# Kernel optimization log

Hardware: AMD Instinct MI355X
Metric: run time of the kernel (lower is better)

The kernel has to match this reference:

```python
import jax, jax.numpy as jnp
import numpy as np
from jax import lax

THD = 0.8  # Lowe ratio-test threshold (module init kwarg `thd`)


def setup_inputs() -> dict:
    key = jax.random.key(0)
    k1, k2 = jax.random.split(key)
    desc1 = jax.random.normal(k1, (16384, 128), dtype=jnp.float32)
    desc2 = jax.random.normal(k2, (16384, 128), dtype=jnp.float32)
    return {"desc1": desc1, "desc2": desc2}


def _cdist(a, b):
    # Euclidean pairwise distances, (B1, B2), same math as torch.cdist(p=2)
    sq_a = jnp.sum(a * a, axis=-1, keepdims=True)          # (B1, 1)
    sq_b = jnp.sum(b * b, axis=-1)                          # (B2,)
    d2 = sq_a + sq_b - 2.0 * (a @ b.T)                      # (B1, B2)
    return jnp.sqrt(jnp.maximum(d2, 0.0))


def reference(desc1, desc2):
    cost = _cdist(desc1, desc2)                             # (B1, B2)
    # two smallest distances per row
    neg_vals, idxs_in_2 = lax.top_k(-cost, 2)               # (B1, 2) each
    vals = -neg_vals
    ratio = vals[:, 0] / vals[:, 1]                         # (B1,)
    mask = ratio <= THD                                     # (B1,) bool
    # jit-compatible padded outputs: masked-out rows carry 0 distance; the
    # boolean mask selects the valid (idxs_in1, idxs_in2) match rows, which is
    # the compaction torch does with boolean indexing.
    match_dists = jnp.where(mask, ratio, 0.0)               # (B1,)
    idxs_in1 = jnp.arange(desc1.shape[0], dtype=jnp.int32)
    matches_idxs = jnp.stack([idxs_in1, idxs_in_2[:, 0].astype(jnp.int32)], axis=1)  # (B1, 2)
    return match_dists, matches_idxs, mask
```

## Files before the change

### kernel.cpp

```cpp
#include <hip/hip_runtime.h>
#include <math.h>
#include <float.h>
#include <stdint.h>


typedef __attribute__((ext_vector_type(4))) float     f32x4;
typedef __attribute__((ext_vector_type(8))) _Float16  half8;

#define D_     128
#define BM_    256
#define BN_    32
#define CS_    8
#define PARTS_ 8

__device__ __forceinline__ void gload_lds16(const void* g, void* l) {
  auto gp = (const __attribute__((address_space(1))) unsigned int*)(uintptr_t)g;
  auto lp = (__attribute__((address_space(3))) unsigned int*)(uintptr_t)l;
  __builtin_amdgcn_global_load_lds(gp, lp, 16, 0, 0);
}

__global__ void convert_kernel(const float* __restrict__ d1, const float* __restrict__ d2,
                               _Float16* __restrict__ Ahi, _Float16* __restrict__ Alo,
                               _Float16* __restrict__ BhiP, _Float16* __restrict__ BloP,
                               float* __restrict__ sq, int B) {
  int i = blockIdx.x * blockDim.x + threadIdx.x;
  int total = B * 16;
  if (i >= 2 * total) return;
  bool isB = i >= total;
  int j    = isB ? i - total : i;
  int desc = j >> 4;
  int seg  = j & 15;
  const float* src = (isB ? d2 : d1) + (size_t)desc * D_ + seg * 8;
  float4 v0 = *(const float4*)(src);
  float4 v1 = *(const float4*)(src + 4);
  half8 hv, lv;
  float e[8] = {v0.x, v0.y, v0.z, v0.w, v1.x, v1.y, v1.z, v1.w};
  float ss = 0.f;
  #pragma unroll
  for (int q = 0; q < 8; ++q) {
    ss = fmaf(e[q], e[q], ss);
    _Float16 h = (_Float16)e[q];
    _Float16 l = (_Float16)(e[q] - (float)h);
    if (isB) { h = (_Float16)(-2.0f) * h; l = (_Float16)(-2.0f) * l; }
    hv[q] = h; lv[q] = l;
  }
  #pragma unroll
  for (int off = 8; off > 0; off >>= 1) ss += __shfl_xor(ss, off, 64);
  if (seg == 0) sq[(isB ? B : 0) + desc] = ss;

  if (!isB) {
    *(half8*)(Ahi + (size_t)desc * D_ + seg * 8) = hv;
    *(half8*)(Alo + (size_t)desc * D_ + seg * 8) = lv;
  } else {
    int t   = desc >> 5, cloc = desc & 31;
    int nf  = cloc >> 4, c15  = cloc & 15;
    int kk  = seg >> 2,  gq   = seg & 3;
    size_t off = (size_t)t * 4096 + kk * 1024 + nf * 512 + gq * 128 + c15 * 8;
    *(half8*)(BhiP + off) = hv;
    *(half8*)(BloP + off) = lv;
  }
}

__global__ __launch_bounds__(256, 2)
void nn_mfma(const _Float16* __restrict__ Ahi, const _Float16* __restrict__ Alo,
             const _Float16* __restrict__ BhiP, const _Float16* __restrict__ BloP,
             const float* __restrict__ sqb,
             float* __restrict__ p_d0, float* __restrict__ p_d1,
             int* __restrict__ p_j0, int B) {
  extern __shared__ char smem[];
  float* sq_lds = (float*)(smem + 65536);
  const int tid  = threadIdx.x;
  const int lane = tid & 63;
  const int wid  = tid >> 6;
  const int l15  = lane & 15;
  const int g    = lane >> 4;

  const int nrb   = B / BM_;
  const int rb    = blockIdx.x % nrb;
  const int cspl  = blockIdx.x / nrb;
  const int i0    = rb * BM_;
  const int ntile = (B / CS_) / BN_;
  const int tile0 = cspl * ntile;

  half8 ah[4][4], al[4][4];
  #pragma unroll
  for (int mf = 0; mf < 4; ++mf) {
    int row = i0 + wid * 64 + mf * 16 + l15;
    const _Float16* pa = Ahi + (size_t)row * D_ + g * 8;
    const _Float16* pl = Alo + (size_t)row * D_ + g * 8;
    #pragma unroll
    for (int kk = 0; kk < 4; ++kk) {
      ah[mf][kk] = *(const half8*)(pa + kk * 32);
      al[mf][kk] = *(const half8*)(pl + kk * 32);
    }
  }

  {
    const float* sqs = sqb + cspl * 2048;
    #pragma unroll
    for (int e = 0; e < 2; ++e) {
      int idx = tid + e * 256;
      float4 v = ((const float4*)sqs)[idx];
      ((float4*)sq_lds)[idx] = v;
    }
  }

  const _Float16* srcW = ((wid < 2) ? BhiP : BloP)
                       + (size_t)tile0 * 4096 + (wid & 1) * 2048 + lane * 8;
  char* ldsW = smem + (wid >> 1) * 8192 + (wid & 1) * 4096;
  auto stage = [&](int slotbase, int t) {
    const _Float16* s = srcW + (size_t)t * 4096;
    char* l = ldsW + slotbase;
    #pragma unroll
    for (int e = 0; e < 4; ++e) gload_lds16(s + e * 512, l + e * 1024);
  };

  float best0[16], best1[16]; int bj[16];
  #pragma unroll
  for (int s = 0; s < 16; ++s) { best0[s] = FLT_MAX; best1[s] = FLT_MAX; bj[s] = 0x7fffffff; }

  const int colg0 = tile0 * BN_ + l15;

  auto tilecomp = [&](int t, int sb) {
    float sjc0 = sq_lds[t * 32 + l15];
    float sjc1 = sq_lds[t * 32 + 16 + l15];
    f32x4 acc[4][2];
    __builtin_amdgcn_s_setprio(1);
    #pragma unroll
    for (int kk = 0; kk < 4; ++kk) {
      half8 bh[2], bl[2];
      #pragma unroll
      for (int nf = 0; nf < 2; ++nf) {
        bh[nf] = *(const half8*)(smem + sb + kk * 2048 + nf * 1024 + lane * 16);
        bl[nf] = *(const half8*)(smem + sb + 8192 + kk * 2048 + nf * 1024 + lane * 16);
      }
      #pragma unroll
      for (int mf = 0; mf < 4; ++mf)
        #pragma unroll
        for (int nf = 0; nf < 2; ++nf) {
          if (kk == 0) {
            float sj = nf ? sjc1 : sjc0;
            f32x4 c0 = {sj, sj, sj, sj};
            acc[mf][nf] = __builtin_amdgcn_mfma_f32_16x16x32_f16(ah[mf][0], bh[nf], c0, 0, 0, 0);
          } else {
            acc[mf][nf] = __builtin_amdgcn_mfma_f32_16x16x32_f16(ah[mf][kk], bh[nf], acc[mf][nf], 0, 0, 0);
          }
        }
      #pragma unroll
      for (int mf = 0; mf < 4; ++mf)
        #pragma unroll
        for (int nf = 0; nf < 2; ++nf)
          acc[mf][nf] = __builtin_amdgcn_mfma_f32_16x16x32_f16(ah[mf][kk], bl[nf], acc[mf][nf], 0, 0, 0);
      #pragma unroll
      for (int mf = 0; mf < 4; ++mf)
        #pragma unroll
        for (int nf = 0; nf < 2; ++nf)
          acc[mf][nf] = __builtin_amdgcn_mfma_f32_16x16x32_f16(al[mf][kk], bh[nf], acc[mf][nf], 0, 0, 0);
    }
    __builtin_amdgcn_s_setprio(0);

    #pragma unroll
    for (int nf = 0; nf < 2; ++nf) {
      int colg = colg0 + t * BN_ + nf * 16;
      #pragma unroll
      for (int mf = 0; mf < 4; ++mf)
        #pragma unroll
        for (int r = 0; r < 4; ++r) {
          int s = mf * 4 + r;
          float v = acc[mf][nf][r];
          best1[s] = __builtin_amdgcn_fmed3f(v, best0[s], best1[s]);
          bool lt0 = v < best0[s];
          best0[s] = fminf(v, best0[s]);
          bj[s]    = lt0 ? colg : bj[s];
        }
    }
  };

  stage(0, 0);
  stage(16384, 1);
  asm volatile("s_waitcnt vmcnt(0)" ::: "memory");
  asm volatile("s_waitcnt lgkmcnt(0)" ::: "memory");
  __builtin_amdgcn_s_barrier();
  asm volatile("" ::: "memory");

  const int nper = ntile / 2;
  for (int p = 0; p < nper; ++p) {
    const int sbcur = (p & 1) * 32768;
    if (p + 1 < nper) {
      stage(sbcur ^ 32768, 2 * p + 2);
      stage((sbcur ^ 32768) + 16384, 2 * p + 3);
    }

    tilecomp(2 * p,     sbcur);
    tilecomp(2 * p + 1, sbcur + 16384);

    asm volatile("s_waitcnt vmcnt(0)" ::: "memory");
    __builtin_amdgcn_s_barrier();
    asm volatile("" ::: "memory");
  }

  #pragma unroll
  for (int off = 1; off < 16; off <<= 1) {
    #pragma unroll
    for (int s = 0; s < 16; ++s) {
      float e0 = __shfl_xor(best0[s], off, 64);
      float e1 = __shfl_xor(best1[s], off, 64);
      int   f0 = __shfl_xor(bj[s],    off, 64);
      if (e0 < best0[s] || (e0 == best0[s] && f0 < bj[s])) {
        best1[s] = fminf(best0[s], e1);
        best0[s] = e0;
        bj[s]    = f0;
      } else {
        best1[s] = fminf(best1[s], e0);
      }
    }
  }

  if (l15 == 0) {
    #pragma unroll
    for (int s = 0; s < 16; ++s) {
      int mf = s >> 2, r = s & 3;
      int row = i0 + wid * 64 + mf * 16 + g * 4 + r;
      p_d0[row * PARTS_ + cspl] = best0[s];
      p_d1[row * PARTS_ + cspl] = best1[s];
      p_j0[row * PARTS_ + cspl] = bj[s];
    }
  }
}

__global__ void nn_final(const float* __restrict__ sqa,
                         const float* __restrict__ p_d0,
                         const float* __restrict__ p_d1,
                         const int* __restrict__ p_j0,
                         float* __restrict__ out, int B) {
  int row = blockIdx.x * blockDim.x + threadIdx.x;
  if (row >= B) return;
  float d0 = FLT_MAX, d1 = FLT_MAX;
  int j0 = 0x7fffffff;
  for (int cs = 0; cs < PARTS_; ++cs) {
    float e0 = p_d0[row * PARTS_ + cs];
    float e1 = p_d1[row * PARTS_ + cs];
    int   f0 = p_j0[row * PARTS_ + cs];
    if (e0 < d0 || (e0 == d0 && f0 < j0)) {
      d1 = fminf(d0, e1);
      d0 = e0;
      j0 = f0;
    } else {
      d1 = fminf(d1, e0);
    }
  }
  float sa = sqa[row];
  float v0 = sqrtf(fmaxf(sa + d0, 0.f));
  float v1 = sqrtf(fmaxf(sa + d1, 0.f));
  float ratio = v0 / v1;
  bool m = (ratio <= 0.8f);
  out[row]             = m ? ratio : 0.f;
  out[B + row * 2]     = (float)row;
  out[B + row * 2 + 1] = (float)j0;
  out[3 * B + row]     = m ? 1.f : 0.f;
}

extern "C" void kernel_launch(void* const* d_in, const int* in_sizes, int n_in,
                              void* d_out, int out_size, void* d_ws, size_t ws_size,
                              hipStream_t stream) {
  const float* d1 = (const float*)d_in[0];
  const float* d2 = (const float*)d_in[1];
  const int B = in_sizes[0] / D_;

  float* ws   = (float*)d_ws;
  float* sqa  = ws;
  float* sqb  = ws + B;
  float* p_d0 = ws + 2 * B;
  float* p_d1 = ws + 10 * B;
  int*   p_j0 = (int*)(ws + 18 * B);
  _Float16* Ahi  = (_Float16*)(ws + 26 * B);
  _Float16* Alo  = Ahi + (size_t)B * D_;
  _Float16* BhiP = Alo + (size_t)B * D_;
  _Float16* BloP = BhiP + (size_t)B * D_;

  int ngroups = 2 * B * 16;
  convert_kernel<<<(ngroups + 255) / 256, 256, 0, stream>>>(d1, d2, Ahi, Alo, BhiP, BloP, sqa, B);

  hipFuncSetAttribute((const void*)nn_mfma,
                      hipFuncAttributeMaxDynamicSharedMemorySize, 73728);
  nn_mfma<<<(B / BM_) * CS_, 256, 73728, stream>>>(Ahi, Alo, BhiP, BloP, sqb,
                                                   p_d0, p_d1, p_j0, B);

  nn_final<<<(B + 255) / 256, 256, 0, stream>>>(sqa, p_d0, p_d1, p_j0, (float*)d_out, B);
}
```

Baseline: 173.9 us.

## Use triple-buffered single-tile LDS pipeline and load half of B-lo directly

Moves from double-buffered pairs of tiles to a three-slot ring of single tiles, prefetching two tiles ahead and waiting on partial vmcnt rather than draining all loads. Only 12 KB per tile is staged through LDS; the upper half of the B-lo fragments is read straight from global memory into registers each iteration. LDS use per block drops from 72 KB to 44 KB, which leaves room for more resident blocks per CU. The trade-off is an extra global load in the inner loop that may stall, and correctness now depends on the vmcnt(3) accounting matching three async loads per stage.

```diff
diff --git a/kernel.cpp b/kernel.cpp
--- a/kernel.cpp
+++ b/kernel.cpp
@@ -68,7 +68,7 @@
              float* __restrict__ p_d0, float* __restrict__ p_d1,
              int* __restrict__ p_j0, int B) {
   extern __shared__ char smem[];
-  float* sq_lds = (float*)(smem + 65536);
+  float* sq_lds = (float*)(smem + 36864);
   const int tid  = threadIdx.x;
   const int lane = tid & 63;
   const int wid  = tid >> 6;
@@ -79,8 +79,8 @@
   const int rb    = blockIdx.x % nrb;
   const int cspl  = blockIdx.x / nrb;
   const int i0    = rb * BM_;
-  const int ntile = (B / CS_) / BN_;
-  const int tile0 = cspl * ntile;
+  const int niter = (B / CS_) / BN_;
+  const int tile0 = cspl * niter;
 
   half8 ah[4][4], al[4][4];
   #pragma unroll
@@ -105,14 +105,15 @@
     }
   }
 
-  const _Float16* srcW = ((wid < 2) ? BhiP : BloP)
-                       + (size_t)tile0 * 4096 + (wid & 1) * 2048 + lane * 8;
-  char* ldsW = smem + (wid >> 1) * 8192 + (wid & 1) * 4096;
   auto stage = [&](int slotbase, int t) {
-    const _Float16* s = srcW + (size_t)t * 4096;
-    char* l = ldsW + slotbase;
-    #pragma unroll
-    for (int e = 0; e < 4; ++e) gload_lds16(s + e * 512, l + e * 1024);
+    const size_t tb = (size_t)(tile0 + t) * 4096;
+    #pragma unroll
+    for (int e = 0; e < 3; ++e) {
+      int c = wid * 3 + e;
+      const _Float16* s = (c < 8) ? (BhiP + tb + c * 512 + lane * 8)
+                                  : (BloP + tb + (c - 8) * 512 + lane * 8);
+      gload_lds16(s, smem + slotbase + c * 1024);
+    }
   };
 
   float best0[16], best1[16]; int bj[16];
@@ -121,9 +122,28 @@
 
   const int colg0 = tile0 * BN_ + l15;
 
-  auto tilecomp = [&](int t, int sb) {
-    float sjc0 = sq_lds[t * 32 + l15];
-    float sjc1 = sq_lds[t * 32 + 16 + l15];
+  stage(0, 0);
+  stage(12288, 1);
+  asm volatile("s_waitcnt vmcnt(3)" ::: "memory");
+  asm volatile("s_waitcnt lgkmcnt(0)" ::: "memory");
+  __builtin_amdgcn_s_barrier();
+  asm volatile("" ::: "memory");
+
+  int bcur = 0, bstage = 24576;
+  for (int it = 0; it < niter; ++it) {
+    const _Float16* blsrc = BloP + (size_t)(tile0 + it) * 4096 + lane * 8;
+    half8 blr[2][2];
+    #pragma unroll
+    for (int dk = 0; dk < 2; ++dk)
+      #pragma unroll
+      for (int nf = 0; nf < 2; ++nf)
+        blr[dk][nf] = *(const half8*)(blsrc + (2 + dk) * 1024 + nf * 512);
+
+    if (it + 2 < niter) stage(bstage, it + 2);
+
+    float sjc0 = sq_lds[it * 32 + l15];
+    float sjc1 = sq_lds[it * 32 + 16 + l15];
+
     f32x4 acc[4][2];
     __builtin_amdgcn_s_setprio(1);
     #pragma unroll
@@ -131,8 +151,11 @@
       half8 bh[2], bl[2];
       #pragma unroll
       for (int nf = 0; nf < 2; ++nf) {
-        bh[nf] = *(const half8*)(smem + sb + kk * 2048 + nf * 1024 + lane * 16);
-        bl[nf] = *(const half8*)(smem + sb + 8192 + kk * 2048 + nf * 1024 + lane * 16);
+        bh[nf] = *(const half8*)(smem + bcur + (kk * 2 + nf) * 1024 + lane * 16);
+        if (kk < 2)
+          bl[nf] = *(const half8*)(smem + bcur + 8192 + (kk * 2 + nf) * 1024 + lane * 16);
+        else
+          bl[nf] = blr[kk - 2][nf];
       }
       #pragma unroll
       for (int mf = 0; mf < 4; ++mf)
@@ -161,42 +184,27 @@
 
     #pragma unroll
     for (int nf = 0; nf < 2; ++nf) {
-      int colg = colg0 + t * BN_ + nf * 16;
+      int colg = colg0 + it * BN_ + nf * 16;
       #pragma unroll
       for (int mf = 0; mf < 4; ++mf)
         #pragma unroll
         for (int r = 0; r < 4; ++r) {
           int s = mf * 4 + r;
-          float v = acc[mf][nf][r];
-          best1[s] = __builtin_amdgcn_fmed3f(v, best0[s], best1[s]);
-          bool lt0 = v < best0[s];
-          best0[s] = fminf(v, best0[s]);
+          float t = acc[mf][nf][r];
+          best1[s] = __builtin_amdgcn_fmed3f(t, best0[s], best1[s]);
+          bool lt0 = t < best0[s];
+          best0[s] = fminf(t, best0[s]);
           bj[s]    = lt0 ? colg : bj[s];
         }
     }
-  };
-
-  stage(0, 0);
-  stage(16384, 1);
-  asm volatile("s_waitcnt vmcnt(0)" ::: "memory");
-  asm volatile("s_waitcnt lgkmcnt(0)" ::: "memory");
-  __builtin_amdgcn_s_barrier();
-  asm volatile("" ::: "memory");
-
-  const int nper = ntile / 2;
-  for (int p = 0; p < nper; ++p) {
-    const int sbcur = (p & 1) * 32768;
-    if (p + 1 < nper) {
-      stage(sbcur ^ 32768, 2 * p + 2);
-      stage((sbcur ^ 32768) + 16384, 2 * p + 3);
-    }
-
-    tilecomp(2 * p,     sbcur);
-    tilecomp(2 * p + 1, sbcur + 16384);
-
-    asm volatile("s_waitcnt vmcnt(0)" ::: "memory");
+
+    if (it + 2 < niter) asm volatile("s_waitcnt vmcnt(3)" ::: "memory");
+    else                asm volatile("s_waitcnt vmcnt(0)" ::: "memory");
     __builtin_amdgcn_s_barrier();
     asm volatile("" ::: "memory");
+
+    bcur   = (bcur   == 24576) ? 0 : bcur   + 12288;
+    bstage = (bstage == 24576) ? 0 : bstage + 12288;
   }
 
   #pragma unroll
@@ -282,8 +290,8 @@
   convert_kernel<<<(ngroups + 255) / 256, 256, 0, stream>>>(d1, d2, Ahi, Alo, BhiP, BloP, sqa, B);
 
   hipFuncSetAttribute((const void*)nn_mfma,
-                      hipFuncAttributeMaxDynamicSharedMemorySize, 73728);
-  nn_mfma<<<(B / BM_) * CS_, 256, 73728, stream>>>(Ahi, Alo, BhiP, BloP, sqb,
+                      hipFuncAttributeMaxDynamicSharedMemorySize, 45056);
+  nn_mfma<<<(B / BM_) * CS_, 256, 45056, stream>>>(Ahi, Alo, BhiP, BloP, sqb,
                                                    p_d0, p_d1, p_j0, B);
 
   nn_final<<<(B + 255) / 256, 256, 0, stream>>>(sqa, p_d0, p_d1, p_j0, (float*)d_out, B);
```

Result: slower. 198.1 us (+13.9%).
